# Performance work log

Hardware: AMD Instinct MI355X
Metric: run time of the kernel (lower is better)

## Reference

```python
import jax, jax.numpy as jnp
import numpy as np

DIM_Q = 1024
DIM_K = 1024
DIM_V = 1024


def setup_inputs() -> dict:
    key = jax.random.key(0)
    kx, kq, kk, kv = jax.random.split(key, 4)
    x = jax.random.normal(kx, (4, 2048, DIM_Q), dtype=jnp.float32)
    # torch nn.Linear weights: [out_features, in_features], y = x @ W.T
    scale = 1.0 / np.sqrt(DIM_Q)
    Wq = jax.random.uniform(kq, (DIM_K, DIM_Q), dtype=jnp.float32, minval=-scale, maxval=scale)
    Wk = jax.random.uniform(kk, (DIM_K, DIM_Q), dtype=jnp.float32, minval=-scale, maxval=scale)
    Wv = jax.random.uniform(kv, (DIM_V, DIM_Q), dtype=jnp.float32, minval=-scale, maxval=scale)
    return {"x": x, "Wq": Wq, "Wk": Wk, "Wv": Wv}


def reference(x, Wq, Wk, Wv):
    # q, k: [b, s, dim_k]; v: [b, s, dim_v]
    q = jnp.einsum('bsd,kd->bsk', x, Wq)
    k = jnp.einsum('bsd,kd->bsk', x, Wk)
    v = jnp.einsum('bsd,vd->bsv', x, Wv)
    norm_fact = 1.0 / jnp.sqrt(jnp.asarray(DIM_K, dtype=x.dtype))
    score = jnp.einsum('bik,bjk->bij', q, k) * norm_fact  # [b, s, s]
    score = jax.nn.softmax(score, axis=-1)
    att = jnp.einsum('bij,bjv->biv', score, v)
    att = att + v  # is_residual=True
    return att
```

## Files before the change

### kernel.cpp

```cpp
#include <hip/hip_runtime.h>
#include <hip/hip_bf16.h>

using bf16 = __hip_bfloat16;
typedef __attribute__((ext_vector_type(8))) short short8;
typedef __attribute__((ext_vector_type(4))) float floatx4;
typedef __attribute__((ext_vector_type(8))) int int8v;

__device__ __forceinline__ void async_ld16(const void* g, void* l) {
  __builtin_amdgcn_global_load_lds((const __attribute__((address_space(1))) void*)g,
                                   (__attribute__((address_space(3))) void*)l, 16, 0, 0);
}

__device__ __forceinline__ int pk4_fp8(float a, float b, float c, float d) {
  int v = __builtin_amdgcn_cvt_pk_fp8_f32(a, b, 0, false);
  return __builtin_amdgcn_cvt_pk_fp8_f32(c, d, v, true);
}

__device__ __forceinline__ int8v ld_frag16(const unsigned char* lo, const unsigned char* hi) {
  int4 l0 = *(const int4*)lo, h0 = *(const int4*)hi;
  int8v v;
  v[0] = l0.x; v[1] = l0.y; v[2] = l0.z; v[3] = l0.w;
  v[4] = h0.x; v[5] = h0.y; v[6] = h0.z; v[7] = h0.w;
  return v;
}


__device__ __forceinline__ void gemm_core(const bf16* __restrict__ At,
                                          const bf16* __restrict__ Bt,
                                          int K, bf16* lA, bf16* lB,
                                          floatx4 acc[4][4]) {
  const int tid  = threadIdx.x;
  const int w    = tid >> 6;
  const int lane = tid & 63;
  const int subM = (w >> 1) * 64;
  const int subN = (w & 1) * 64;
  const int fr   = lane & 15;
  const int fq   = lane >> 4;

  int srow[4], scol[4], sdst[4];
#pragma unroll
  for (int q = 0; q < 4; ++q) {
    int p = q * 256 + w * 64 + lane;
    int r = p >> 3;
    int j = (p & 7) ^ (r & 7);
    srow[q] = r;
    scol[q] = j * 8;
    sdst[q] = (q * 256 + w * 64) * 8;
  }
  int offA[2][4], offB[2][4];
#pragma unroll
  for (int kc = 0; kc < 2; ++kc)
#pragma unroll
    for (int i = 0; i < 4; ++i) {
      int rA = subM + i * 16 + fr;
      offA[kc][i] = (rA * 8 + ((kc * 4 + fq) ^ (rA & 7))) * 8;
      int rB = subN + i * 16 + fr;
      offB[kc][i] = (rB * 8 + ((kc * 4 + fq) ^ (rB & 7))) * 8;
    }

  floatx4 zero = {0.f, 0.f, 0.f, 0.f};
#pragma unroll
  for (int i = 0; i < 4; ++i)
#pragma unroll
    for (int j = 0; j < 4; ++j) acc[i][j] = zero;

  for (int k0 = 0; k0 < K; k0 += 64) {
    __syncthreads();
#pragma unroll
    for (int q = 0; q < 4; ++q) {
      async_ld16(At + (size_t)srow[q] * K + k0 + scol[q], lA + sdst[q]);
      async_ld16(Bt + (size_t)srow[q] * K + k0 + scol[q], lB + sdst[q]);
    }
    __syncthreads();
#pragma unroll
    for (int kc = 0; kc < 2; ++kc) {
      short8 a[4], b[4];
#pragma unroll
      for (int i = 0; i < 4; ++i) a[i] = *(const short8*)(lA + offA[kc][i]);
#pragma unroll
      for (int j = 0; j < 4; ++j) b[j] = *(const short8*)(lB + offB[kc][j]);
#pragma unroll
      for (int i = 0; i < 4; ++i)
#pragma unroll
        for (int j = 0; j < 4; ++j)
          acc[i][j] = __builtin_amdgcn_mfma_f32_16x16x32_bf16(a[i], b[j], acc[i][j], 0, 0, 0);
    }
  }
}

__device__ __forceinline__ void gemm_core_f8(const unsigned char* __restrict__ At,
                                             const unsigned char* __restrict__ Bt,
                                             int K, unsigned char* lA, unsigned char* lB,
                                             floatx4 acc[4][4]) {
  const int tid  = threadIdx.x;
  const int w    = tid >> 6;
  const int lane = tid & 63;
  const int subM = (w >> 1) * 64;
  const int subN = (w & 1) * 64;
  const int fr   = lane & 15;
  const int fq   = lane >> 4;

  int srow[4], scol[4], sdst[4];
#pragma unroll
  for (int q = 0; q < 4; ++q) {
    int p = q * 256 + w * 64 + lane;
    int r = p >> 3;
    int j = (p & 7) ^ (r & 7) ^ ((r & 8) >> 1);
    srow[q] = r;
    scol[q] = j * 16;
    sdst[q] = (q * 256 + w * 64) * 16;
  }
  int offA[2][4], offB[2][4];
#pragma unroll
  for (int h = 0; h < 2; ++h)
#pragma unroll
    for (int i = 0; i < 4; ++i) {
      int rA = subM + i * 16 + fr;
      offA[h][i] = rA * 128 + (((fq * 2 + h) ^ (rA & 7) ^ ((rA & 8) >> 1)) * 16);
      int rB = subN + i * 16 + fr;
      offB[h][i] = rB * 128 + (((fq * 2 + h) ^ (rB & 7) ^ ((rB & 8) >> 1)) * 16);
    }

  floatx4 zero = {0.f, 0.f, 0.f, 0.f};
#pragma unroll
  for (int i = 0; i < 4; ++i)
#pragma unroll
    for (int j = 0; j < 4; ++j) acc[i][j] = zero;

  for (int k0 = 0; k0 < K; k0 += 128) {
    __syncthreads();
#pragma unroll
    for (int q = 0; q < 4; ++q) {
      async_ld16(At + (size_t)srow[q] * K + k0 + scol[q], lA + sdst[q]);
      async_ld16(Bt + (size_t)srow[q] * K + k0 + scol[q], lB + sdst[q]);
    }
    __syncthreads();
    int8v a[4], b[4];
#pragma unroll
    for (int i = 0; i < 4; ++i) a[i] = ld_frag16(lA + offA[0][i], lA + offA[1][i]);
#pragma unroll
    for (int j = 0; j < 4; ++j) b[j] = ld_frag16(lB + offB[0][j], lB + offB[1][j]);
#pragma unroll
    for (int i = 0; i < 4; ++i)
#pragma unroll
      for (int j = 0; j < 4; ++j)
        acc[i][j] = __builtin_amdgcn_mfma_scale_f32_16x16x128_f8f6f4(
            a[i], b[j], acc[i][j], 0, 0, 0, 0x7F7F7F7F, 0, 0x7F7F7F7F);
  }
}

__device__ __forceinline__ void gemm_core_f8_v2(const unsigned char* __restrict__ At,
                                                const unsigned char* __restrict__ Bt,
                                                int K, unsigned char* lA, unsigned char* lB,
                                                floatx4 acc[4][8]) {
  const int tid  = threadIdx.x;
  const int w    = tid >> 6;
  const int lane = tid & 63;
  const int subM = (w >> 1) * 64;
  const int subN = (w & 1) * 128;
  const int fr   = lane & 15;
  const int fq   = lane >> 4;

  int srowA[4], scolA[4], sdstA[4];
#pragma unroll
  for (int q = 0; q < 4; ++q) {
    int p = q * 256 + w * 64 + lane;
    int r = p >> 3;
    int j = (p & 7) ^ (r & 7) ^ ((r & 8) >> 1);
    srowA[q] = r; scolA[q] = j * 16; sdstA[q] = (q * 256 + w * 64) * 16;
  }
  int srowB[8], scolB[8], sdstB[8];
#pragma unroll
  for (int q = 0; q < 8; ++q) {
    int p = q * 256 + w * 64 + lane;
    int r = p >> 3;
    int j = (p & 7) ^ (r & 7) ^ ((r & 8) >> 1);
    srowB[q] = r; scolB[q] = j * 16; sdstB[q] = (q * 256 + w * 64) * 16;
  }
  int offA[2][4], offB[2][8];
#pragma unroll
  for (int h = 0; h < 2; ++h) {
#pragma unroll
    for (int i = 0; i < 4; ++i) {
      int rA = subM + i * 16 + fr;
      offA[h][i] = rA * 128 + (((fq * 2 + h) ^ (rA & 7) ^ ((rA & 8) >> 1)) * 16);
    }
#pragma unroll
    for (int j = 0; j < 8; ++j) {
      int rB = subN + j * 16 + fr;
      offB[h][j] = rB * 128 + (((fq * 2 + h) ^ (rB & 7) ^ ((rB & 8) >> 1)) * 16);
    }
  }

  floatx4 zero = {0.f, 0.f, 0.f, 0.f};
#pragma unroll
  for (int i = 0; i < 4; ++i)
#pragma unroll
    for (int j = 0; j < 8; ++j) acc[i][j] = zero;

  for (int k0 = 0; k0 < K; k0 += 128) {
    __syncthreads();
#pragma unroll
    for (int q = 0; q < 4; ++q)
      async_ld16(At + (size_t)srowA[q] * K + k0 + scolA[q], lA + sdstA[q]);
#pragma unroll
    for (int q = 0; q < 8; ++q)
      async_ld16(Bt + (size_t)srowB[q] * K + k0 + scolB[q], lB + sdstB[q]);
    __syncthreads();
    int8v a[4];
#pragma unroll
    for (int i = 0; i < 4; ++i) a[i] = ld_frag16(lA + offA[0][i], lA + offA[1][i]);
#pragma unroll
    for (int j = 0; j < 8; ++j) {
      int8v bf = ld_frag16(lB + offB[0][j], lB + offB[1][j]);
#pragma unroll
      for (int i = 0; i < 4; ++i)
        acc[i][j] = __builtin_amdgcn_mfma_scale_f32_16x16x128_f8f6f4(
            a[i], bf, acc[i][j], 0, 0, 0, 0x7F7F7F7F, 0, 0x7F7F7F7F);
    }
  }
}

__global__ __launch_bounds__(256, 2) void proj_gemm(
    const bf16* __restrict__ Xbf, const bf16* __restrict__ Wvbf, bf16* __restrict__ Vbf,
    const unsigned char* __restrict__ X8, const unsigned char* __restrict__ Wq8,
    const unsigned char* __restrict__ Wk8,
    unsigned char* __restrict__ Qf8, unsigned char* __restrict__ Kf8) {
  __shared__ __align__(16) char lds[49152];
  const int id = blockIdx.x;
  const int tid = threadIdx.x, w = tid >> 6, lane = tid & 63;
  const int fr = lane & 15, fq = lane >> 4;

  if (id < 512) {
    const int r = id & 7, g = id >> 3;
    const int ty = r * 8 + (g & 7), tx = g >> 3;
    bf16* lA = (bf16*)lds;
    bf16* lB = (bf16*)(lds + 16384);
    floatx4 acc[4][4];
    gemm_core(Xbf + (size_t)ty * 128 * 1024, Wvbf + (size_t)tx * 128 * 1024,
              1024, lA, lB, acc);
    const int subM = (w >> 1) * 64, subN = (w & 1) * 64;
    const int rowBase = ty * 128 + subM;
    const int colBase = tx * 128 + subN;
#pragma unroll
    for (int i = 0; i < 4; ++i)
#pragma unroll
      for (int j = 0; j < 4; ++j)
#pragma unroll
        for (int rr = 0; rr < 4; ++rr) {
          int row = rowBase + i * 16 + fq * 4 + rr;
          int col = colBase + j * 16 + fr;
          Vbf[(size_t)row * 1024 + col] = __float2bfloat16(acc[i][j][rr]);
        }
  } else {
    const int local = id - 512;
    const int z = local >> 8, lid = local & 255;
    const int r = lid & 7, g = lid >> 3;
    const int ty = r * 8 + (g & 7);
    const int tx = g >> 3;
    unsigned char* lA = (unsigned char*)lds;
    unsigned char* lB = (unsigned char*)(lds + 16384);
    floatx4 acc[4][8];
    gemm_core_f8_v2(X8 + (size_t)ty * 128 * 1024,
                    (z == 0 ? Wq8 : Wk8) + (size_t)tx * 256 * 1024, 1024, lA, lB, acc);
    unsigned char* dst = (z == 0) ? Qf8 : Kf8;
    const int subM = (w >> 1) * 64, subN = (w & 1) * 128;
    const int rowBase = ty * 128 + subM;
    const int colBase = tx * 256 + subN;
#pragma unroll
    for (int i = 0; i < 4; ++i)
#pragma unroll
      for (int rr = 0; rr < 4; ++rr) {
        int row = rowBase + i * 16 + fq * 4 + rr;
        unsigned int p0 = (unsigned int)pk4_fp8(acc[i][0][rr], acc[i][1][rr],
                                                acc[i][2][rr], acc[i][3][rr]);
        unsigned int p1 = (unsigned int)pk4_fp8(acc[i][4][rr], acc[i][5][rr],
                                                acc[i][6][rr], acc[i][7][rr]);
        *(unsigned int*)&dst[(size_t)row * 1024 + colBase + fr * 4] = p0;
        *(unsigned int*)&dst[(size_t)row * 1024 + colBase + 64 + fr * 4] = p1;
      }
  }
}

__global__ __launch_bounds__(256, 2) void mid_kernel(
    const unsigned char* __restrict__ Qf8, const unsigned char* __restrict__ Kf8,
    unsigned char* __restrict__ S8, float* __restrict__ l,
    const bf16* __restrict__ Vbf, unsigned char* __restrict__ Vt8) {
  __shared__ __align__(16) char lds[49152];
  const int id = blockIdx.x;
  const int t = threadIdx.x;

  if (id < 512) {
    const int r = id & 7, g = id >> 3;
    const int b = g >> 4;
    const int rem = g & 15;
    const int ty = r * 2 + (rem & 1);
    const int tx = rem >> 1;
    unsigned char* lA = (unsigned char*)lds;
    unsigned char* lB = (unsigned char*)(lds + 16384);
    floatx4 acc[4][8];
    gemm_core_f8_v2(Qf8 + (size_t)b * 2048 * 1024 + (size_t)ty * 128 * 1024,
                    Kf8 + (size_t)b * 2048 * 1024 + (size_t)tx * 256 * 1024,
                    1024, lA, lB, acc);
    const int w = t >> 6, lane = t & 63;
    const int subM = (w >> 1) * 64, subN = (w & 1) * 128;
    const int fr = lane & 15, fq = lane >> 4;
    const int rowBase = ty * 128 + subM;
    const int colBase = tx * 256 + subN;
    unsigned char* Sb = S8 + (size_t)b * 2048 * 2048;
    float* lb = l + (size_t)b * 2048;
#pragma unroll
    for (int i = 0; i < 4; ++i)
#pragma unroll
      for (int rr = 0; rr < 4; ++rr) {
        int row = rowBase + i * 16 + fq * 4 + rr;
        unsigned int p0 = (unsigned int)pk4_fp8(
            __expf(acc[i][0][rr] * 0.03125f), __expf(acc[i][1][rr] * 0.03125f),
            __expf(acc[i][2][rr] * 0.03125f), __expf(acc[i][3][rr] * 0.03125f));
        unsigned int p1 = (unsigned int)pk4_fp8(
            __expf(acc[i][4][rr] * 0.03125f), __expf(acc[i][5][rr] * 0.03125f),
            __expf(acc[i][6][rr] * 0.03125f), __expf(acc[i][7][rr] * 0.03125f));
        *(unsigned int*)&Sb[(size_t)row * 2048 + colBase + fr * 4] = p0;
        *(unsigned int*)&Sb[(size_t)row * 2048 + colBase + 64 + fr * 4] = p1;
        float psum = __builtin_amdgcn_cvt_f32_fp8(p0, 0) + __builtin_amdgcn_cvt_f32_fp8(p0, 1) +
                     __builtin_amdgcn_cvt_f32_fp8(p0, 2) + __builtin_amdgcn_cvt_f32_fp8(p0, 3) +
                     __builtin_amdgcn_cvt_f32_fp8(p1, 0) + __builtin_amdgcn_cvt_f32_fp8(p1, 1) +
                     __builtin_amdgcn_cvt_f32_fp8(p1, 2) + __builtin_amdgcn_cvt_f32_fp8(p1, 3);
        psum += __shfl_xor(psum, 1, 64);
        psum += __shfl_xor(psum, 2, 64);
        psum += __shfl_xor(psum, 4, 64);
        psum += __shfl_xor(psum, 8, 64);
        if (fr == 0) atomicAdd(&lb[row], psum);
      }
  } else {
    const int t2 = id - 512;
    const int b = t2 >> 9, rem = t2 & 511;
    const int xs = rem & 31, yv = rem >> 5;
    const int s0 = xs * 64, v0 = yv * 64;
    short(*tile)[72] = (short(*)[72])lds;
#pragma unroll
    for (int i = 0; i < 2; ++i) {
      int c = t + i * 256;
      int row = c >> 3, cj = c & 7;
      *(short8*)&tile[row][cj * 8] =
          *(const short8*)&Vbf[((size_t)(b * 2048 + s0 + row)) * 1024 + v0 + cj * 8];
    }
    __syncthreads();
    const int vrow = t >> 2, sq = t & 3;
#pragma unroll
    for (int hc = 0; hc < 2; ++hc) {
      float f[8];
#pragma unroll
      for (int e = 0; e < 8; ++e) {
        int p = sq * 16 + hc * 8 + e;
        int s = (p & 3) * 16 + (p >> 2);
        short sh = tile[s][vrow];
        f[e] = __bfloat162float(*(bf16*)&sh);
      }
      uint2 packed;
      packed.x = (unsigned int)pk4_fp8(f[0], f[1], f[2], f[3]);
      packed.y = (unsigned int)pk4_fp8(f[4], f[5], f[6], f[7]);
      *(uint2*)&Vt8[((size_t)(b * 1024 + v0 + vrow)) * 2048 + s0 + sq * 16 + hc * 8] = packed;
    }
  }
}

__global__ __launch_bounds__(256) void pv_gemm(const unsigned char* __restrict__ S8,
                                               const unsigned char* __restrict__ Vt8,
                                               const bf16* __restrict__ Vbf,
                                               const float* __restrict__ l,
                                               float* __restrict__ out) {
  __shared__ __align__(16) char lds[32768];
  unsigned char* lA = (unsigned char*)lds;
  unsigned char* lB = (unsigned char*)(lds + 16384);
  const int id = blockIdx.x;
  const int r = id & 7, g = id >> 3;
  const int b = g >> 4;
  const int rem = g & 15;
  const int ty = r * 2 + (rem & 1);
  const int tx = rem >> 1;

  floatx4 acc[4][4];
  gemm_core_f8(S8 + (size_t)b * 2048 * 2048 + (size_t)ty * 128 * 2048,
               Vt8 + (size_t)b * 1024 * 2048 + (size_t)tx * 128 * 2048,
               2048, lA, lB, acc);

  const int tid = threadIdx.x, w = tid >> 6, lane = tid & 63;
  const int subM = (w >> 1) * 64, subN = (w & 1) * 64;
  const int fr = lane & 15, fq = lane >> 4;
  const int rowBase = ty * 128 + subM;
  const int colBase = tx * 128 + subN;
  const float* lb = l + (size_t)b * 2048;
#pragma unroll
  for (int i = 0; i < 4; ++i)
#pragma unroll
    for (int rr = 0; rr < 4; ++rr) {
      int row = rowBase + i * 16 + fq * 4 + rr;
      float inv = 1.0f / lb[row];
#pragma unroll
      for (int j = 0; j < 4; ++j) {
        int col = colBase + j * 16 + fr;
        size_t oi = ((size_t)b * 2048 + row) * 1024 + col;
        out[oi] = acc[i][j][rr] * inv + __bfloat162float(Vbf[oi]);
      }
    }
}

__global__ void cast_all(const float* __restrict__ x, const float* __restrict__ wq,
                         const float* __restrict__ wk, const float* __restrict__ wv,
                         bf16* __restrict__ Xbf, unsigned char* __restrict__ X8,
                         unsigned char* __restrict__ Wq8, unsigned char* __restrict__ Wk8,
                         bf16* __restrict__ Wvbf, float* __restrict__ l) {
  const int blk = blockIdx.x;
  const int t = threadIdx.x;
  if (blk < 8192) {
    int i = blk * 256 + t;
    float4 f = ((const float4*)x)[i];
    bf16 tmp[4] = {__float2bfloat16(f.x), __float2bfloat16(f.y),
                   __float2bfloat16(f.z), __float2bfloat16(f.w)};
    ((ushort4*)Xbf)[i] = *(const ushort4*)tmp;
    ((unsigned int*)X8)[i] = (unsigned int)pk4_fp8(f.x, f.y, f.z, f.w);
  } else if (blk < 10240) {
    const float* src = (blk < 9216) ? wq : wk;
    unsigned char* dst = (blk < 9216) ? Wq8 : Wk8;
    int i = ((blk - 8192) & 1023) * 256 + t;
    float4 f = ((const float4*)src)[i];
    ((unsigned int*)dst)[i] = (unsigned int)pk4_fp8(f.x, f.y, f.z, f.w);
  } else if (blk < 11264) {
    int i = (blk - 10240) * 256 + t;
    float4 f = ((const float4*)wv)[i];
    bf16 tmp[4] = {__float2bfloat16(f.x), __float2bfloat16(f.y),
                   __float2bfloat16(f.z), __float2bfloat16(f.w)};
    ((ushort4*)Wvbf)[i] = *(const ushort4*)tmp;
  } else {
    int i = (blk - 11264) * 256 + t;
    ((float4*)l)[i] = make_float4(0.f, 0.f, 0.f, 0.f);
  }
}

extern "C" void kernel_launch(void* const* d_in, const int* in_sizes, int n_in,
                              void* d_out, int out_size, void* d_ws, size_t ws_size,
                              hipStream_t stream) {
  const float* x  = (const float*)d_in[0];
  const float* Wq = (const float*)d_in[1];
  const float* Wk = (const float*)d_in[2];
  const float* Wv = (const float*)d_in[3];
  float* out = (float*)d_out;

  char* ws = (char*)d_ws;
  bf16* Xbf = (bf16*)ws;                   ws += (size_t)8192 * 1024 * 2;
  unsigned char* X8 = (unsigned char*)ws;  ws += (size_t)8192 * 1024;
  unsigned char* Wq8 = (unsigned char*)ws; ws += (size_t)1024 * 1024;
  unsigned char* Wk8 = (unsigned char*)ws; ws += (size_t)1024 * 1024;
  bf16* Wvbf = (bf16*)ws;                  ws += (size_t)1024 * 1024 * 2;
  unsigned char* Qf8 = (unsigned char*)ws; ws += (size_t)8192 * 1024;
  unsigned char* Kf8 = (unsigned char*)ws; ws += (size_t)8192 * 1024;
  bf16* Vbf = (bf16*)ws;                   ws += (size_t)8192 * 1024 * 2;
  unsigned char* Vt8 = (unsigned char*)ws; ws += (size_t)4 * 1024 * 2048;
  unsigned char* S8  = (unsigned char*)ws; ws += (size_t)4 * 2048 * 2048;
  float* l = (float*)ws;                   ws += (size_t)8192 * 4;

  cast_all<<<11272, 256, 0, stream>>>(x, Wq, Wk, Wv, Xbf, X8, Wq8, Wk8, Wvbf, l);
  proj_gemm<<<1024, 256, 0, stream>>>(Xbf, Wvbf, Vbf, X8, Wq8, Wk8, Qf8, Kf8);
  mid_kernel<<<2560, 256, 0, stream>>>(Qf8, Kf8, S8, l, Vbf, Vt8);
  pv_gemm<<<512, 256, 0, stream>>>(S8, Vt8, Vbf, l, out);
}
```

Measured before the change: 176.3 us.

## Fuse all stages into one persistent cooperative kernel with grid syncs

Adds a persistent cooperative kernel of 512 blocks that runs the casts, the projections, the QK^T/exp stage, the V transpose and the PV GEMM in sequence, separated by grid-wide barriers. It falls back to the old four-kernel path if occupancy is too low or the cooperative launch fails. The aim is to remove launch gaps and tail effects between kernels. In exchange the fused path uses the smaller 128x128 FP8 core instead of the wider v2 tiles, runs a fixed 512-block grid, and adds grid-barrier overhead.

Result: no change. 177.2 us (+0.5%).

```diff
diff --git a/kernel.cpp b/kernel.cpp
--- a/kernel.cpp
+++ b/kernel.cpp
@@ -1,5 +1,8 @@
 #include <hip/hip_runtime.h>
 #include <hip/hip_bf16.h>
+#include <hip/hip_cooperative_groups.h>
+
+namespace cg = cooperative_groups;
 
 using bf16 = __hip_bfloat16;
 typedef __attribute__((ext_vector_type(8))) short short8;
@@ -23,7 +26,6 @@
   v[4] = h0.x; v[5] = h0.y; v[6] = h0.z; v[7] = h0.w;
   return v;
 }
-
 
 __device__ __forceinline__ void gemm_core(const bf16* __restrict__ At,
                                           const bf16* __restrict__ Bt,
@@ -221,6 +223,196 @@
   }
 }
 
+__global__ __launch_bounds__(256, 2) void fused_all(
+    const float* __restrict__ x, const float* __restrict__ wq,
+    const float* __restrict__ wk, const float* __restrict__ wv,
+    bf16* __restrict__ Xbf, unsigned char* __restrict__ X8,
+    unsigned char* __restrict__ Wq8, unsigned char* __restrict__ Wk8,
+    bf16* __restrict__ Wvbf, bf16* __restrict__ Vbf,
+    unsigned char* __restrict__ Qf8, unsigned char* __restrict__ Kf8,
+    unsigned char* __restrict__ S8, unsigned char* __restrict__ Vt8,
+    float* __restrict__ l, float* __restrict__ out) {
+  __shared__ __align__(16) char lds[32768];
+  cg::grid_group grid = cg::this_grid();
+  const int rb = blockIdx.x;
+  const int t = threadIdx.x;
+  const int w = t >> 6, lane = t & 63;
+  const int fr = lane & 15, fq = lane >> 4;
+
+  for (int blk = rb; blk < 11272; blk += 512) {
+    if (blk < 8192) {
+      int i = blk * 256 + t;
+      float4 f = ((const float4*)x)[i];
+      bf16 tmp[4] = {__float2bfloat16(f.x), __float2bfloat16(f.y),
+                     __float2bfloat16(f.z), __float2bfloat16(f.w)};
+      ((ushort4*)Xbf)[i] = *(const ushort4*)tmp;
+      ((unsigned int*)X8)[i] = (unsigned int)pk4_fp8(f.x, f.y, f.z, f.w);
+    } else if (blk < 10240) {
+      const float* src = (blk < 9216) ? wq : wk;
+      unsigned char* dst = (blk < 9216) ? Wq8 : Wk8;
+      int i = ((blk - 8192) & 1023) * 256 + t;
+      float4 f = ((const float4*)src)[i];
+      ((unsigned int*)dst)[i] = (unsigned int)pk4_fp8(f.x, f.y, f.z, f.w);
+    } else if (blk < 11264) {
+      int i = (blk - 10240) * 256 + t;
+      float4 f = ((const float4*)wv)[i];
+      bf16 tmp[4] = {__float2bfloat16(f.x), __float2bfloat16(f.y),
+                     __float2bfloat16(f.z), __float2bfloat16(f.w)};
+      ((ushort4*)Wvbf)[i] = *(const ushort4*)tmp;
+    } else {
+      int i = (blk - 11264) * 256 + t;
+      ((float4*)l)[i] = make_float4(0.f, 0.f, 0.f, 0.f);
+    }
+  }
+  __threadfence();
+  grid.sync();
+
+  {
+    const int r = rb & 7, g = rb >> 3;
+    const int ty = r * 8 + (g & 7), tx = g >> 3;
+    floatx4 acc[4][4];
+    gemm_core(Xbf + (size_t)ty * 128 * 1024, Wvbf + (size_t)tx * 128 * 1024,
+              1024, (bf16*)lds, (bf16*)(lds + 16384), acc);
+    const int subM = (w >> 1) * 64, subN = (w & 1) * 64;
+    const int rowBase = ty * 128 + subM;
+    const int colBase = tx * 128 + subN;
+#pragma unroll
+    for (int i = 0; i < 4; ++i)
+#pragma unroll
+      for (int j = 0; j < 4; ++j)
+#pragma unroll
+        for (int rr = 0; rr < 4; ++rr) {
+          int row = rowBase + i * 16 + fq * 4 + rr;
+          int col = colBase + j * 16 + fr;
+          Vbf[(size_t)row * 1024 + col] = __float2bfloat16(acc[i][j][rr]);
+        }
+  }
+#pragma unroll 1
+  for (int z = 0; z < 2; ++z) {
+    const int r = rb & 7, g = rb >> 3;
+    const int ty = r * 8 + (g & 7), tx = g >> 3;
+    floatx4 acc[4][4];
+    gemm_core_f8(X8 + (size_t)ty * 128 * 1024,
+                 (z == 0 ? Wq8 : Wk8) + (size_t)tx * 128 * 1024, 1024,
+                 (unsigned char*)lds, (unsigned char*)(lds + 16384), acc);
+    unsigned char* dst = (z == 0) ? Qf8 : Kf8;
+    const int subM = (w >> 1) * 64, subN = (w & 1) * 64;
+    const int rowBase = ty * 128 + subM;
+    const int colBase = tx * 128 + subN;
+#pragma unroll
+    for (int i = 0; i < 4; ++i)
+#pragma unroll
+      for (int rr = 0; rr < 4; ++rr) {
+        int row = rowBase + i * 16 + fq * 4 + rr;
+        unsigned int p = (unsigned int)pk4_fp8(acc[i][0][rr], acc[i][1][rr],
+                                               acc[i][2][rr], acc[i][3][rr]);
+        *(unsigned int*)&dst[(size_t)row * 1024 + colBase + fr * 4] = p;
+      }
+  }
+  __threadfence();
+  grid.sync();
+
+#pragma unroll 1
+  for (int q = 0; q < 2; ++q) {
+    const int id = rb + q * 512;
+    const int r = id & 7, g = id >> 3;
+    const int b = g >> 5;
+    const int rem = g & 31;
+    const int ty = r * 2 + (rem & 1);
+    const int tx = rem >> 1;
+    floatx4 acc[4][4];
+    gemm_core_f8(Qf8 + (size_t)b * 2048 * 1024 + (size_t)ty * 128 * 1024,
+                 Kf8 + (size_t)b * 2048 * 1024 + (size_t)tx * 128 * 1024, 1024,
+                 (unsigned char*)lds, (unsigned char*)(lds + 16384), acc);
+    const int subM = (w >> 1) * 64, subN = (w & 1) * 64;
+    const int rowBase = ty * 128 + subM;
+    const int colBase = tx * 128 + subN;
+    unsigned char* Sb = S8 + (size_t)b * 2048 * 2048;
+    float* lb = l + (size_t)b * 2048;
+#pragma unroll
+    for (int i = 0; i < 4; ++i)
+#pragma unroll
+      for (int rr = 0; rr < 4; ++rr) {
+        int row = rowBase + i * 16 + fq * 4 + rr;
+        unsigned int p = (unsigned int)pk4_fp8(
+            __expf(acc[i][0][rr] * 0.03125f), __expf(acc[i][1][rr] * 0.03125f),
+            __expf(acc[i][2][rr] * 0.03125f), __expf(acc[i][3][rr] * 0.03125f));
+        *(unsigned int*)&Sb[(size_t)row * 2048 + colBase + fr * 4] = p;
+        float psum = __builtin_amdgcn_cvt_f32_fp8(p, 0) + __builtin_amdgcn_cvt_f32_fp8(p, 1) +
+                     __builtin_amdgcn_cvt_f32_fp8(p, 2) + __builtin_amdgcn_cvt_f32_fp8(p, 3);
+        psum += __shfl_xor(psum, 1, 64);
+        psum += __shfl_xor(psum, 2, 64);
+        psum += __shfl_xor(psum, 4, 64);
+        psum += __shfl_xor(psum, 8, 64);
+        if (fr == 0) atomicAdd(&lb[row], psum);
+      }
+  }
+#pragma unroll 1
+  for (int q = 0; q < 4; ++q) {
+    const int t2 = rb * 4 + q;
+    const int b = t2 >> 9, rem = t2 & 511;
+    const int xs = rem & 31, yv = rem >> 5;
+    const int s0 = xs * 64, v0 = yv * 64;
+    short(*tile)[72] = (short(*)[72])lds;
+    __syncthreads();
+#pragma unroll
+    for (int i = 0; i < 2; ++i) {
+      int c = t + i * 256;
+      int row = c >> 3, cj = c & 7;
+      *(short8*)&tile[row][cj * 8] =
+          *(const short8*)&Vbf[((size_t)(b * 2048 + s0 + row)) * 1024 + v0 + cj * 8];
+    }
+    __syncthreads();
+    const int vrow = t >> 2, sq = t & 3;
+#pragma unroll
+    for (int hc = 0; hc < 2; ++hc) {
+      float f[8];
+#pragma unroll
+      for (int e = 0; e < 8; ++e) {
+        int p = sq * 16 + hc * 8 + e;
+        int s = (p & 3) * 16 + (p >> 2);
+        short sh = tile[s][vrow];
+        f[e] = __bfloat162float(*(bf16*)&sh);
+      }
+      uint2 packed;
+      packed.x = (unsigned int)pk4_fp8(f[0], f[1], f[2], f[3]);
+      packed.y = (unsigned int)pk4_fp8(f[4], f[5], f[6], f[7]);
+      *(uint2*)&Vt8[((size_t)(b * 1024 + v0 + vrow)) * 2048 + s0 + sq * 16 + hc * 8] = packed;
+    }
+  }
+  __threadfence();
+  grid.sync();
+
+  {
+    const int r = rb & 7, g = rb >> 3;
+    const int b = g >> 4;
+    const int rem = g & 15;
+    const int ty = r * 2 + (rem & 1);
+    const int tx = rem >> 1;
+    floatx4 acc[4][4];
+    gemm_core_f8(S8 + (size_t)b * 2048 * 2048 + (size_t)ty * 128 * 2048,
+                 Vt8 + (size_t)b * 1024 * 2048 + (size_t)tx * 128 * 2048, 2048,
+                 (unsigned char*)lds, (unsigned char*)(lds + 16384), acc);
+    const int subM = (w >> 1) * 64, subN = (w & 1) * 64;
+    const int rowBase = ty * 128 + subM;
+    const int colBase = tx * 128 + subN;
+    const float* lb = l + (size_t)b * 2048;
+#pragma unroll
+    for (int i = 0; i < 4; ++i)
+#pragma unroll
+      for (int rr = 0; rr < 4; ++rr) {
+        int row = rowBase + i * 16 + fq * 4 + rr;
+        float inv = 1.0f / lb[row];
+#pragma unroll
+        for (int j = 0; j < 4; ++j) {
+          int col = colBase + j * 16 + fr;
+          size_t oi = ((size_t)b * 2048 + row) * 1024 + col;
+          out[oi] = acc[i][j][rr] * inv + __bfloat162float(Vbf[oi]);
+        }
+      }
+  }
+}
+
 __global__ __launch_bounds__(256, 2) void proj_gemm(
     const bf16* __restrict__ Xbf, const bf16* __restrict__ Wvbf, bf16* __restrict__ Vbf,
     const unsigned char* __restrict__ X8, const unsigned char* __restrict__ Wq8,
@@ -234,11 +426,9 @@
   if (id < 512) {
     const int r = id & 7, g = id >> 3;
     const int ty = r * 8 + (g & 7), tx = g >> 3;
-    bf16* lA = (bf16*)lds;
-    bf16* lB = (bf16*)(lds + 16384);
     floatx4 acc[4][4];
     gemm_core(Xbf + (size_t)ty * 128 * 1024, Wvbf + (size_t)tx * 128 * 1024,
-              1024, lA, lB, acc);
+              1024, (bf16*)lds, (bf16*)(lds + 16384), acc);
     const int subM = (w >> 1) * 64, subN = (w & 1) * 64;
     const int rowBase = ty * 128 + subM;
     const int colBase = tx * 128 + subN;
@@ -258,11 +448,10 @@
     const int r = lid & 7, g = lid >> 3;
     const int ty = r * 8 + (g & 7);
     const int tx = g >> 3;
-    unsigned char* lA = (unsigned char*)lds;
-    unsigned char* lB = (unsigned char*)(lds + 16384);
     floatx4 acc[4][8];
     gemm_core_f8_v2(X8 + (size_t)ty * 128 * 1024,
-                    (z == 0 ? Wq8 : Wk8) + (size_t)tx * 256 * 1024, 1024, lA, lB, acc);
+                    (z == 0 ? Wq8 : Wk8) + (size_t)tx * 256 * 1024, 1024,
+                    (unsigned char*)lds, (unsigned char*)(lds + 16384), acc);
     unsigned char* dst = (z == 0) ? Qf8 : Kf8;
     const int subM = (w >> 1) * 64, subN = (w & 1) * 128;
     const int rowBase = ty * 128 + subM;
@@ -296,12 +485,10 @@
     const int rem = g & 15;
     const int ty = r * 2 + (rem & 1);
     const int tx = rem >> 1;
-    unsigned char* lA = (unsigned char*)lds;
-    unsigned char* lB = (unsigned char*)(lds + 16384);
     floatx4 acc[4][8];
     gemm_core_f8_v2(Qf8 + (size_t)b * 2048 * 1024 + (size_t)ty * 128 * 1024,
-                    Kf8 + (size_t)b * 2048 * 1024 + (size_t)tx * 256 * 1024,
-                    1024, lA, lB, acc);
+                    Kf8 + (size_t)b * 2048 * 1024 + (size_t)tx * 256 * 1024, 1024,
+                    (unsigned char*)lds, (unsigned char*)(lds + 16384), acc);
     const int w = t >> 6, lane = t & 63;
     const int subM = (w >> 1) * 64, subN = (w & 1) * 128;
     const int fr = lane & 15, fq = lane >> 4;
@@ -371,8 +558,6 @@
                                                const float* __restrict__ l,
                                                float* __restrict__ out) {
   __shared__ __align__(16) char lds[32768];
-  unsigned char* lA = (unsigned char*)lds;
-  unsigned char* lB = (unsigned char*)(lds + 16384);
   const int id = blockIdx.x;
   const int r = id & 7, g = id >> 3;
   const int b = g >> 4;
@@ -382,8 +567,8 @@
 
   floatx4 acc[4][4];
   gemm_core_f8(S8 + (size_t)b * 2048 * 2048 + (size_t)ty * 128 * 2048,
-               Vt8 + (size_t)b * 1024 * 2048 + (size_t)tx * 128 * 2048,
-               2048, lA, lB, acc);
+               Vt8 + (size_t)b * 1024 * 2048 + (size_t)tx * 128 * 2048, 2048,
+               (unsigned char*)lds, (unsigned char*)(lds + 16384), acc);
 
   const int tid = threadIdx.x, w = tid >> 6, lane = tid & 63;
   const int subM = (w >> 1) * 64, subN = (w & 1) * 64;
@@ -453,13 +638,23 @@
   unsigned char* Wq8 = (unsigned char*)ws; ws += (size_t)1024 * 1024;
   unsigned char* Wk8 = (unsigned char*)ws; ws += (size_t)1024 * 1024;
   bf16* Wvbf = (bf16*)ws;                  ws += (size_t)1024 * 1024 * 2;
+  bf16* Vbf = (bf16*)ws;                   ws += (size_t)8192 * 1024 * 2;
   unsigned char* Qf8 = (unsigned char*)ws; ws += (size_t)8192 * 1024;
   unsigned char* Kf8 = (unsigned char*)ws; ws += (size_t)8192 * 1024;
-  bf16* Vbf = (bf16*)ws;                   ws += (size_t)8192 * 1024 * 2;
+  unsigned char* S8  = (unsigned char*)ws; ws += (size_t)4 * 2048 * 2048;
   unsigned char* Vt8 = (unsigned char*)ws; ws += (size_t)4 * 1024 * 2048;
-  unsigned char* S8  = (unsigned char*)ws; ws += (size_t)4 * 2048 * 2048;
   float* l = (float*)ws;                   ws += (size_t)8192 * 4;
 
+  int nb = 0;
+  hipError_t qerr = hipOccupancyMaxActiveBlocksPerMultiprocessor(&nb, fused_all, 256, 0);
+  if (qerr == hipSuccess && nb >= 2) {
+    const float *xa = x, *wqa = Wq, *wka = Wk, *wva = Wv;
+    void* args[] = {&xa, &wqa, &wka, &wva, &Xbf, &X8, &Wq8, &Wk8, &Wvbf, &Vbf,
+                    &Qf8, &Kf8, &S8, &Vt8, &l, &out};
+    hipError_t lerr = hipLaunchCooperativeKernel((const void*)fused_all, dim3(512),
+                                                 dim3(256), args, 0, stream);
+    if (lerr == hipSuccess) return;
+  }
   cast_all<<<11272, 256, 0, stream>>>(x, Wq, Wk, Wv, Xbf, X8, Wq8, Wk8, Wvbf, l);
   proj_gemm<<<1024, 256, 0, stream>>>(Xbf, Wvbf, Vbf, X8, Wq8, Wk8, Qf8, Kf8);
   mid_kernel<<<2560, 256, 0, stream>>>(Qf8, Kf8, S8, l, Vbf, Vt8);
```
